# Kernel tuning notes

Measured on AMD Instinct MI355X. Metric: run time of the kernel, lower is better.

The kernel has to match this reference:

```python
import jax, jax.numpy as jnp
import numpy as np

N = 100000   # nodes
E = 1600000  # edges (avg degree 16)
IN = 24
HID = 128
OUT = 12


def setup_inputs() -> dict:
    key = jax.random.key(0)
    ks = jax.random.split(key, 16)
    s = 0.05
    return {
        "inputs": jax.random.normal(ks[0], (N, IN), jnp.float32),
        "src": jax.random.randint(ks[1], (E,), 0, N),
        "dst": jax.random.randint(ks[2], (E,), 0, N),
        "e_w": jax.random.uniform(ks[3], (E, 1), jnp.float32),
        "snorm_n": jax.random.uniform(ks[4], (N, 1), jnp.float32),
        "snorm_e": jax.random.uniform(ks[5], (E, 1), jnp.float32),
        "W_emb": jax.random.normal(ks[6], (IN, HID), jnp.float32) * s,
        "b_emb": jnp.zeros((HID,), jnp.float32),
        "W_self1": jax.random.normal(ks[7], (HID, HID), jnp.float32) * s,
        "W1": jax.random.normal(ks[8], (HID, HID), jnp.float32) * s,
        "b1": jnp.zeros((HID,), jnp.float32),
        "W_self2": jax.random.normal(ks[9], (HID, HID), jnp.float32) * s,
        "W2": jax.random.normal(ks[10], (HID, HID), jnp.float32) * s,
        "b2": jnp.zeros((HID,), jnp.float32),
        "W_fc": jax.random.normal(ks[11], (HID, OUT), jnp.float32) * s,
        "b_fc": jnp.zeros((OUT,), jnp.float32),
    }


def _degrees(src, dst):
    out_deg = jnp.clip(jnp.zeros((N,), jnp.float32).at[src].add(1.0), 1.0)
    in_deg = jnp.clip(jnp.zeros((N,), jnp.float32).at[dst].add(1.0), 1.0)
    return out_deg, in_deg


def _gcn_layer(h, src, dst, e_w, out_deg, in_deg, W_self, W, b):
    # self transform (no bias)
    h_s = h @ W_self
    # source-side symmetric norm, edge-weighted message, sum-aggregate at dst
    feat = h * (out_deg ** -0.5)[:, None]          # [N, H]
    m = feat[src] * e_w                            # [E, H]  u_mul_e
    agg = jax.ops.segment_sum(m, dst, num_segments=N)  # [N, H] sum reduce
    h2 = (agg @ W + b) * (in_deg ** -0.5)[:, None]
    return h_s + h2


def reference(inputs, src, dst, e_w, snorm_n, snorm_e,
              W_emb, b_emb, W_self1, W1, b1, W_self2, W2, b2, W_fc, b_fc):
    out_deg, in_deg = _degrees(src, dst)
    h = inputs @ W_emb + b_emb
    h = jax.nn.relu(_gcn_layer(h, src, dst, e_w, out_deg, in_deg, W_self1, W1, b1))
    h = jax.nn.relu(_gcn_layer(h, src, dst, e_w, out_deg, in_deg, W_self2, W2, b2))
    return h @ W_fc + b_fc
```

## Files before the change

kernel.cpp:

```cpp
#include <hip/hip_runtime.h>

#define NN 100000
#define EE 1600000
#define IN_F 24
#define HID 128
#define OUT_F 12
#define HC 256
#define LBLK 128

#define NBKT 782
#define PA_BLKS 512
#define PA_EPB 3125

#define EMB_B 2048
#define PREP_B 264
#define K1_GRID (PA_BLKS + EMB_B + PREP_B)

typedef unsigned char u8;
typedef unsigned short u16;
typedef unsigned int u32;

using short8 = __attribute__((ext_vector_type(8))) short;
using f32x4  = __attribute__((ext_vector_type(4))) float;

__device__ __forceinline__ float bf2f(u16 h) {
  return __uint_as_float(((u32)h) << 16);
}
__device__ __forceinline__ u16 f2bf(float f) {
  u32 u = __float_as_uint(f);
  u32 r = (u + 0x7FFFu + ((u >> 16) & 1u)) >> 16;
  return (u16)r;
}
__device__ __forceinline__ float inv_sqrt_cnt(int c) {
  if (c < 1) c = 1;
  return 1.0f / sqrtf((float)c);
}

__device__ __forceinline__ void emb_body(int eb, const float* __restrict__ inputs,
                                         const float* __restrict__ W_emb,
                                         const float* __restrict__ b_emb,
                                         u16* __restrict__ hcat, float* smemW) {
  int t = threadIdx.x;
  float* Wls = smemW;
  float* bls = smemW + IN_F * HID;
  for (int i = t; i < IN_F * HID; i += 256) Wls[i] = W_emb[i];
  if (t < HID) bls[t] = b_emb[t];
  __syncthreads();
  int c = t & 127;
  int sub = t >> 7;
  for (int node = eb * 2 + sub; node < NN; node += EMB_B * 2) {
    const float* xr = inputs + (size_t)node * IN_F;
    float acc = bls[c];
    #pragma unroll
    for (int k = 0; k < IN_F; ++k) acc = fmaf(xr[k], Wls[k * HID + c], acc);
    hcat[(size_t)node * HC + c] = f2bf(acc);
  }
}

__device__ __forceinline__ void prep_body(int pb,
    const float* __restrict__ Ws1, const float* __restrict__ W1m,
    const float* __restrict__ Ws2, const float* __restrict__ W2m,
    const float* __restrict__ Wfc,
    u16* __restrict__ WT1, u16* __restrict__ WT2, u16* __restrict__ WfcT) {
  int idx = pb * 256 + (int)threadIdx.x;
  if (idx < 65536) {
    int layer = idx >> 15;
    int rem = idx & 32767;
    int n = rem >> 8, k = rem & 255;
    const float* A = layer ? Ws2 : Ws1;
    const float* B = layer ? W2m : W1m;
    float v = (k < HID) ? A[(size_t)k * HID + n] : B[(size_t)(k - HID) * HID + n];
    (layer ? WT2 : WT1)[(size_t)n * 256 + k] = f2bf(v);
  } else if (idx < 65536 + 2048) {
    int j = idx - 65536;
    int n = j >> 7, k = j & 127;
    WfcT[(size_t)n * 128 + k] = f2bf(n < OUT_F ? Wfc[(size_t)k * OUT_F + n] : 0.f);
  }
}

__global__ __launch_bounds__(256) void k1(
    const int* __restrict__ src, const int* __restrict__ dst,
    u32* __restrict__ histgD, u32* __restrict__ histgS,
    const float* __restrict__ inputs, const float* __restrict__ W_emb,
    const float* __restrict__ b_emb, u16* __restrict__ hcat,
    const float* __restrict__ Ws1, const float* __restrict__ W1m,
    const float* __restrict__ Ws2, const float* __restrict__ W2m,
    const float* __restrict__ Wfc,
    u16* __restrict__ WT1, u16* __restrict__ WT2, u16* __restrict__ WfcT) {
  __shared__ __align__(16) char sm[13312];
  int b = blockIdx.x, t = threadIdx.x;
  if (b < PA_BLKS) {
    u32* histD = (u32*)sm;
    u32* histS = histD + 1024;
    for (int i = t; i < 2048; i += 256) histD[i] = 0;
    __syncthreads();
    int e0 = b * PA_EPB;
    for (int e = e0 + t; e < e0 + PA_EPB; e += 256) {
      atomicAdd(&histD[dst[e] >> 7], 1u);
      atomicAdd(&histS[src[e] >> 7], 1u);
    }
    __syncthreads();
    for (int i = t; i < 1024; i += 256) {
      histgD[(size_t)b * 1024 + i] = histD[i];
      histgS[(size_t)b * 1024 + i] = histS[i];
    }
  } else if (b < PA_BLKS + EMB_B) {
    emb_body(b - PA_BLKS, inputs, W_emb, b_emb, hcat, (float*)sm);
  } else {
    prep_body(b - PA_BLKS - EMB_B, Ws1, W1m, Ws2, W2m, Wfc, WT1, WT2, WfcT);
  }
}

__global__ __launch_bounds__(256) void k_scan1(u32* __restrict__ histgD,
                                               u32* __restrict__ histgS,
                                               u32* __restrict__ totalsD,
                                               u32* __restrict__ totalsS) {
  __shared__ u32 s[512];
  int b = blockIdx.x, t = threadIdx.x;
  u32* hist = (b < NBKT) ? histgD : histgS;
  u32* tot  = (b < NBKT) ? totalsD : totalsS;
  int k = (b < NBKT) ? b : b - NBKT;
  u32 v0 = hist[(size_t)t * 1024 + k];
  u32 v1 = hist[(size_t)(t + 256) * 1024 + k];
  s[t] = v0; s[t + 256] = v1;
  __syncthreads();
  for (int off = 1; off < 512; off <<= 1) {
    u32 a0 = (t >= off) ? s[t - off] : 0;
    u32 a1 = (t + 256 >= off) ? s[t + 256 - off] : 0;
    __syncthreads();
    s[t] += a0; s[t + 256] += a1;
    __syncthreads();
  }
  hist[(size_t)t * 1024 + k] = s[t] - v0;
  hist[(size_t)(t + 256) * 1024 + k] = s[t + 256] - v1;
  if (t == 255) tot[k] = s[511];
}

__global__ __launch_bounds__(1024) void k_scan2(const u32* __restrict__ totalsD,
                                                const u32* __restrict__ totalsS,
                                                u32* __restrict__ estartD,
                                                u32* __restrict__ sstart) {
  __shared__ u32 s[1024];
  const u32* tot = blockIdx.x ? totalsS : totalsD;
  u32* est       = blockIdx.x ? sstart  : estartD;
  int t = threadIdx.x;
  u32 v = (t < NBKT) ? tot[t] : 0;
  s[t] = v;
  __syncthreads();
  for (int off = 1; off < 1024; off <<= 1) {
    u32 a = (t >= off) ? s[t - off] : 0;
    __syncthreads();
    s[t] += a;
    __syncthreads();
  }
  if (t < NBKT) est[t] = s[t] - v;
  if (t == NBKT - 1) est[NBKT] = s[t];
}

__global__ __launch_bounds__(256) void k_passbS(
    const int* __restrict__ src, const u32* __restrict__ histgS,
    const u32* __restrict__ sstart, u8* __restrict__ lo8) {
  __shared__ u32 cur[1024];
  int pb = blockIdx.x, t = threadIdx.x;
  for (int i = t; i < 1024; i += 256)
    cur[i] = ((i < NBKT) ? sstart[i] : 0u) + histgS[(size_t)pb * 1024 + i];
  __syncthreads();
  int e0 = pb * PA_EPB;
  for (int e = e0 + t; e < e0 + PA_EPB; e += 256) {
    int s = src[e];
    u32 pos = atomicAdd(&cur[s >> 7], 1u);
    lo8[pos] = (u8)(s & 127);
  }
}

__global__ __launch_bounds__(256) void k_countS(const u8* __restrict__ lo8,
                                                const u32* __restrict__ sstart,
                                                float* __restrict__ out_norm) {
  __shared__ u32 cnt[128];
  int k = blockIdx.x, t = threadIdx.x;
  if (t < 128) cnt[t] = 0;
  __syncthreads();
  int e0 = (int)sstart[k], e1 = (int)sstart[k + 1];
  for (int e = e0 + t; e < e1; e += 256) atomicAdd(&cnt[lo8[e]], 1u);
  __syncthreads();
  if (t < 128) {
    int node = k * 128 + t;
    if (node < NN) out_norm[node] = inv_sqrt_cnt((int)cnt[t]);
  }
}

__global__ __launch_bounds__(256) void k_passbD(
    const int* __restrict__ src, const int* __restrict__ dst,
    const float* __restrict__ e_w, const float* __restrict__ out_norm,
    const u32* __restrict__ histgD, const u32* __restrict__ estartD,
    u32* __restrict__ csr_stage, u8* __restrict__ dl8) {
  __shared__ u32 cur[1024];
  int pb = blockIdx.x, t = threadIdx.x;
  for (int i = t; i < 1024; i += 256)
    cur[i] = ((i < NBKT) ? estartD[i] : 0u) + histgD[(size_t)pb * 1024 + i];
  __syncthreads();
  int e0 = pb * PA_EPB;
  for (int e = e0 + t; e < e0 + PA_EPB; e += 256) {
    int s = src[e], d = dst[e];
    float w = e_w[e] * out_norm[s];
    u32 pos = atomicAdd(&cur[d >> 7], 1u);
    csr_stage[pos] = (((u32)f2bf(w)) << 17) | (u32)s;
    dl8[pos] = (u8)(d & 127);
  }
}

__global__ __launch_bounds__(256) void k_reorder(
    const u32* __restrict__ csr_stage, const u8* __restrict__ dl8,
    const u32* __restrict__ estart, u32* __restrict__ csr,
    int* __restrict__ row_start, float* __restrict__ in_norm) {
  __shared__ u32 cnt[128], pfx[128], cur[128];
  int k = blockIdx.x, t = threadIdx.x;
  if (t < 128) cnt[t] = 0;
  __syncthreads();
  int e0 = (int)estart[k], e1 = (int)estart[k + 1];
  for (int e = e0 + t; e < e1; e += 256) atomicAdd(&cnt[dl8[e]], 1u);
  __syncthreads();
  if (t < 128) pfx[t] = cnt[t];
  __syncthreads();
  for (int off = 1; off < 128; off <<= 1) {
    u32 v = (t < 128 && t >= off) ? pfx[t - off] : 0;
    __syncthreads();
    if (t < 128) pfx[t] += v;
    __syncthreads();
  }
  if (t < 128) {
    u32 start = (u32)e0 + pfx[t] - cnt[t];
    cur[t] = start;
    int node = k * 128 + t;
    if (node < NN) {
      row_start[node] = (int)start;
      in_norm[node] = inv_sqrt_cnt((int)cnt[t]);
    }
  }
  if (k == NBKT - 1 && t == 0) row_start[NN] = e1;
  __syncthreads();
  for (int e = e0 + t; e < e1; e += 256) {
    u32 pos = atomicAdd(&cur[dl8[e]], 1u);
    csr[pos] = csr_stage[e];
  }
}

__global__ __launch_bounds__(256) void k_agg(const u16* __restrict__ hcat_in,
                                             const int* __restrict__ row_start,
                                             const float* __restrict__ in_norm,
                                             const u32* __restrict__ csr,
                                             u16* __restrict__ hcat_out) {
  int t = threadIdx.x;
  int node = blockIdx.x * 8 + (t >> 5);
  if (node >= NN) return;
  int lane = t & 31;
  int s0 = row_start[node], s1 = row_start[node + 1];
  float ax = 0.f, ay = 0.f, az = 0.f, aw = 0.f;
  for (int i0 = s0; i0 < s1; i0 += 32) {
    u32 pk = 0;
    if (i0 + lane < s1) pk = csr[i0 + lane];
    int m = s1 - i0; if (m > 32) m = 32;
    for (int j = 0; j < m; ++j) {
      u32 p = __shfl(pk, j, 32);
      float w = bf2f((u16)(p >> 17));
      int sv = (int)(p & 0x1FFFF);
      ushort4 hv = *(const ushort4*)(hcat_in + (size_t)sv * HC + lane * 4);
      ax = fmaf(w, bf2f(hv.x), ax);
      ay = fmaf(w, bf2f(hv.y), ay);
      az = fmaf(w, bf2f(hv.z), az);
      aw = fmaf(w, bf2f(hv.w), aw);
    }
  }
  float inn = in_norm[node];
  ushort4 r;
  r.x = f2bf(ax * inn); r.y = f2bf(ay * inn);
  r.z = f2bf(az * inn); r.w = f2bf(aw * inn);
  *(ushort4*)(hcat_out + (size_t)node * HC + HID + lane * 4) = r;
}

template<int FC>
__global__ __launch_bounds__(512) void k_layer(u16* __restrict__ hcat,
    const u16* __restrict__ WT, const float* __restrict__ bias,
    const float* __restrict__ in_norm,
    const u16* __restrict__ WfcT, const float* __restrict__ b_fc,
    float* __restrict__ out) {
  __shared__ char smem[135168];
  const int t = threadIdx.x;
  const int r0 = blockIdx.x * LBLK;

  #pragma unroll
  for (int i = 0; i < 8; ++i) {
    int boff = i * 8192 + t * 16;
    int row = boff >> 9, col = boff & 511;
    uint4 v = *(const uint4*)(hcat + (size_t)(r0 + row) * HC + (col >> 1));
    *(uint4*)(smem + row * 512 + (col ^ ((row & 7) << 4))) = v;
  }
  #pragma unroll
  for (int i = 0; i < 8; ++i) {
    int boff = i * 8192 + t * 16;
    int row = boff >> 9, col = boff & 511;
    uint4 v = *(const uint4*)(WT + (size_t)row * 256 + (col >> 1));
    *(uint4*)(smem + 65536 + row * 512 + (col ^ ((row & 7) << 4))) = v;
  }
  if (FC && t < 256) {
    int row = t >> 4, col = (t & 15) * 16;
    uint4 v = *(const uint4*)(WfcT + (size_t)row * 128 + (col >> 1));
    *(uint4*)(smem + 131072 + row * 256 + (col ^ ((row & 7) << 4))) = v;
  }
  __syncthreads();

  const int lane = t & 63, w = t >> 6;
  const int l15 = lane & 15, lhi = lane >> 4;

  f32x4 acc[8];
  #pragma unroll
  for (int nf = 0; nf < 8; ++nf) acc[nf] = (f32x4){0.f, 0.f, 0.f, 0.f};

  const int arow = w * 16 + l15;
  const char* pa = smem + arow * 512;
  const int aswz = (arow & 7) << 4;
  #pragma unroll
  for (int ks = 0; ks < 8; ++ks) {
    int kb = ks * 64 + (lhi << 4);
    short8 a = *(const short8*)(pa + (kb ^ aswz));
    #pragma unroll
    for (int nf = 0; nf < 8; ++nf) {
      int brow = nf * 16 + l15;
      short8 bf = *(const short8*)(smem + 65536 + brow * 512 + (kb ^ ((brow & 7) << 4)));
      acc[nf] = __builtin_amdgcn_mfma_f32_16x16x32_bf16(a, bf, acc[nf], 0, 0, 0);
    }
  }

  float bcol[8];
  #pragma unroll
  for (int nf = 0; nf < 8; ++nf) bcol[nf] = bias[nf * 16 + l15];

  if (!FC) {
    #pragma unroll
    for (int r = 0; r < 4; ++r) {
      int grow = r0 + w * 16 + (lhi << 2) + r;
      if (grow < NN) {
        float inn = in_norm[grow];
        #pragma unroll
        for (int nf = 0; nf < 8; ++nf) {
          float v = acc[nf][r] + inn * bcol[nf];
          hcat[(size_t)grow * HC + nf * 16 + l15] = f2bf(fmaxf(v, 0.f));
        }
      }
    }
  } else {
    #pragma unroll
    for (int r = 0; r < 4; ++r) {
      int lrow = w * 16 + (lhi << 2) + r;
      int grow = r0 + lrow;
      float inn = (grow < NN) ? in_norm[grow] : 0.f;
      #pragma unroll
      for (int nf = 0; nf < 8; ++nf) {
        int col = nf * 16 + l15;
        float v = fmaxf(acc[nf][r] + inn * bcol[nf], 0.f);
        *(u16*)(smem + lrow * 256 + ((col * 2) ^ ((lrow & 7) << 4))) = f2bf(v);
      }
    }
    __syncthreads();
    f32x4 a2 = (f32x4){0.f, 0.f, 0.f, 0.f};
    const char* pa2 = smem + (w * 16 + l15) * 256;
    const int as2 = (l15 & 7) << 4;
    #pragma unroll
    for (int ks = 0; ks < 4; ++ks) {
      int kb = ks * 64 + (lhi << 4);
      short8 a = *(const short8*)(pa2 + (kb ^ as2));
      short8 bf = *(const short8*)(smem + 131072 + l15 * 256 + (kb ^ as2));
      a2 = __builtin_amdgcn_mfma_f32_16x16x32_bf16(a, bf, a2, 0, 0, 0);
    }
    if (l15 < OUT_F) {
      float bo = b_fc[l15];
      #pragma unroll
      for (int r = 0; r < 4; ++r) {
        int grow = r0 + w * 16 + (lhi << 2) + r;
        if (grow < NN) out[(size_t)grow * OUT_F + l15] = a2[r] + bo;
      }
    }
  }
}

extern "C" void kernel_launch(void* const* d_in, const int* in_sizes, int n_in,
                              void* d_out, int out_size, void* d_ws, size_t ws_size,
                              hipStream_t stream) {
  (void)in_sizes; (void)n_in; (void)out_size;
  const float* inputs  = (const float*)d_in[0];
  const int*   src     = (const int*)d_in[1];
  const int*   dst     = (const int*)d_in[2];
  const float* e_w     = (const float*)d_in[3];
  const float* W_emb   = (const float*)d_in[6];
  const float* b_emb   = (const float*)d_in[7];
  const float* W_self1 = (const float*)d_in[8];
  const float* W1      = (const float*)d_in[9];
  const float* b1      = (const float*)d_in[10];
  const float* W_self2 = (const float*)d_in[11];
  const float* W2      = (const float*)d_in[12];
  const float* b2      = (const float*)d_in[13];
  const float* W_fc    = (const float*)d_in[14];
  const float* b_fc    = (const float*)d_in[15];
  float* out = (float*)d_out;

  u32* histgD      = (u32*)d_ws;
  u32* histgS      = histgD + (size_t)512 * 1024;
  u32* totalsD     = histgS + (size_t)512 * 1024;
  u32* estartD     = totalsD + 1024;
  u32* totalsS     = estartD + 1024;
  u32* sstart      = totalsS + 1024;
  float* out_norm  = (float*)(sstart + 1024);
  float* in_norm   = out_norm + NN;
  int* row_start   = (int*)(in_norm + NN);
  u8* lo8          = (u8*)(row_start + NN + 4);
  u32* csr_stage   = (u32*)(lo8 + EE);
  u32* csr         = csr_stage + EE;
  u16* hcat        = (u16*)(csr + EE);
  u16* WT1         = hcat + (size_t)NN * HC;
  u16* WT2         = WT1 + 32768;
  u16* WfcT        = WT2 + 32768;

  const size_t NEED = (size_t)2 * 512 * 1024 * 4 + 4096 * 4 + (size_t)(3 * NN + 4) * 4
                      + (size_t)EE * 9 + (size_t)NN * HC * 2 + (2 * 32768 + 2048) * 2;
  if (ws_size < NEED) return;

  hipLaunchKernelGGL(k1, dim3(K1_GRID), dim3(256), 0, stream,
                     src, dst, histgD, histgS, inputs, W_emb, b_emb, hcat,
                     W_self1, W1, W_self2, W2, W_fc, WT1, WT2, WfcT);
  hipLaunchKernelGGL(k_scan1, dim3(2 * NBKT), dim3(256), 0, stream,
                     histgD, histgS, totalsD, totalsS);
  hipLaunchKernelGGL(k_scan2, dim3(2), dim3(1024), 0, stream,
                     totalsD, totalsS, estartD, sstart);
  hipLaunchKernelGGL(k_passbS, dim3(PA_BLKS), dim3(256), 0, stream,
                     src, histgS, sstart, lo8);
  hipLaunchKernelGGL(k_countS, dim3(NBKT), dim3(256), 0, stream, lo8, sstart, out_norm);
  hipLaunchKernelGGL(k_passbD, dim3(PA_BLKS), dim3(256), 0, stream,
                     src, dst, e_w, out_norm, histgD, estartD, csr_stage, lo8);
  hipLaunchKernelGGL(k_reorder, dim3(NBKT), dim3(256), 0, stream,
                     csr_stage, lo8, estartD, csr, row_start, in_norm);
  hipLaunchKernelGGL(k_agg, dim3((NN + 7) / 8), dim3(256), 0, stream,
                     hcat, row_start, in_norm, csr, hcat);
  hipLaunchKernelGGL(k_layer<0>, dim3((NN + LBLK - 1) / LBLK), dim3(512), 0, stream,
                     hcat, WT1, b1, in_norm, WfcT, b_fc, out);
  hipLaunchKernelGGL(k_agg, dim3((NN + 7) / 8), dim3(256), 0, stream,
                     hcat, row_start, in_norm, csr, hcat);
  hipLaunchKernelGGL(k_layer<1>, dim3((NN + LBLK - 1) / LBLK), dim3(512), 0, stream,
                     hcat, WT2, b2, in_norm, WfcT, b_fc, out);
}
```

Baseline: 381.0 us.

## Split concatenated feature buffer into separate h and aggregate arrays; unroll gather

Replaces the interleaved [N,256] hcat buffer, which held h and the aggregate side by side, with two dense [N,128] arrays. The gather in k_agg then reads from a compact array with a 256-byte row stride instead of 512, so gathered rows sit closer together and use cache lines better. The gather loop is also unrolled by four so that several independent row loads are in flight at once. k_layer now loads its two halves from the separate arrays into the same swizzled shared layout, which costs an extra pass of address arithmetic but keeps the matmul unchanged.

```diff
diff --git a/kernel.cpp b/kernel.cpp
--- a/kernel.cpp
+++ b/kernel.cpp
@@ -5,7 +5,6 @@
 #define IN_F 24
 #define HID 128
 #define OUT_F 12
-#define HC 256
 #define LBLK 128
 
 #define NBKT 782
@@ -39,7 +38,7 @@
 __device__ __forceinline__ void emb_body(int eb, const float* __restrict__ inputs,
                                          const float* __restrict__ W_emb,
                                          const float* __restrict__ b_emb,
-                                         u16* __restrict__ hcat, float* smemW) {
+                                         u16* __restrict__ harr, float* smemW) {
   int t = threadIdx.x;
   float* Wls = smemW;
   float* bls = smemW + IN_F * HID;
@@ -53,7 +52,7 @@
     float acc = bls[c];
     #pragma unroll
     for (int k = 0; k < IN_F; ++k) acc = fmaf(xr[k], Wls[k * HID + c], acc);
-    hcat[(size_t)node * HC + c] = f2bf(acc);
+    harr[(size_t)node * HID + c] = f2bf(acc);
   }
 }
 
@@ -82,7 +81,7 @@
     const int* __restrict__ src, const int* __restrict__ dst,
     u32* __restrict__ histgD, u32* __restrict__ histgS,
     const float* __restrict__ inputs, const float* __restrict__ W_emb,
-    const float* __restrict__ b_emb, u16* __restrict__ hcat,
+    const float* __restrict__ b_emb, u16* __restrict__ harr,
     const float* __restrict__ Ws1, const float* __restrict__ W1m,
     const float* __restrict__ Ws2, const float* __restrict__ W2m,
     const float* __restrict__ Wfc,
@@ -105,7 +104,7 @@
       histgS[(size_t)b * 1024 + i] = histS[i];
     }
   } else if (b < PA_BLKS + EMB_B) {
-    emb_body(b - PA_BLKS, inputs, W_emb, b_emb, hcat, (float*)sm);
+    emb_body(b - PA_BLKS, inputs, W_emb, b_emb, harr, (float*)sm);
   } else {
     prep_body(b - PA_BLKS - EMB_B, Ws1, W1m, Ws2, W2m, Wfc, WT1, WT2, WfcT);
   }
@@ -245,11 +244,11 @@
   }
 }
 
-__global__ __launch_bounds__(256) void k_agg(const u16* __restrict__ hcat_in,
+__global__ __launch_bounds__(256) void k_agg(const u16* __restrict__ harr,
                                              const int* __restrict__ row_start,
                                              const float* __restrict__ in_norm,
                                              const u32* __restrict__ csr,
-                                             u16* __restrict__ hcat_out) {
+                                             u16* __restrict__ aggr) {
   int t = threadIdx.x;
   int node = blockIdx.x * 8 + (t >> 5);
   if (node >= NN) return;
@@ -260,26 +259,47 @@
     u32 pk = 0;
     if (i0 + lane < s1) pk = csr[i0 + lane];
     int m = s1 - i0; if (m > 32) m = 32;
-    for (int j = 0; j < m; ++j) {
+    int j = 0;
+    for (; j + 4 <= m; j += 4) {
+      u32 p0 = __shfl(pk, j,     32);
+      u32 p1 = __shfl(pk, j + 1, 32);
+      u32 p2 = __shfl(pk, j + 2, 32);
+      u32 p3 = __shfl(pk, j + 3, 32);
+      ushort4 h0 = *(const ushort4*)(harr + (size_t)(p0 & 0x1FFFF) * HID + lane * 4);
+      ushort4 h1 = *(const ushort4*)(harr + (size_t)(p1 & 0x1FFFF) * HID + lane * 4);
+      ushort4 h2 = *(const ushort4*)(harr + (size_t)(p2 & 0x1FFFF) * HID + lane * 4);
+      ushort4 h3 = *(const ushort4*)(harr + (size_t)(p3 & 0x1FFFF) * HID + lane * 4);
+      float w0 = bf2f((u16)(p0 >> 17));
+      float w1 = bf2f((u16)(p1 >> 17));
+      float w2 = bf2f((u16)(p2 >> 17));
+      float w3 = bf2f((u16)(p3 >> 17));
+      ax = fmaf(w0, bf2f(h0.x), ax); ay = fmaf(w0, bf2f(h0.y), ay);
+      az = fmaf(w0, bf2f(h0.z), az); aw = fmaf(w0, bf2f(h0.w), aw);
+      ax = fmaf(w1, bf2f(h1.x), ax); ay = fmaf(w1, bf2f(h1.y), ay);
+      az = fmaf(w1, bf2f(h1.z), az); aw = fmaf(w1, bf2f(h1.w), aw);
+      ax = fmaf(w2, bf2f(h2.x), ax); ay = fmaf(w2, bf2f(h2.y), ay);
+      az = fmaf(w2, bf2f(h2.z), az); aw = fmaf(w2, bf2f(h2.w), aw);
+      ax = fmaf(w3, bf2f(h3.x), ax); ay = fmaf(w3, bf2f(h3.y), ay);
+      az = fmaf(w3, bf2f(h3.z), az); aw = fmaf(w3, bf2f(h3.w), aw);
+    }
+    for (; j < m; ++j) {
       u32 p = __shfl(pk, j, 32);
       float w = bf2f((u16)(p >> 17));
-      int sv = (int)(p & 0x1FFFF);
-      ushort4 hv = *(const ushort4*)(hcat_in + (size_t)sv * HC + lane * 4);
-      ax = fmaf(w, bf2f(hv.x), ax);
-      ay = fmaf(w, bf2f(hv.y), ay);
-      az = fmaf(w, bf2f(hv.z), az);
-      aw = fmaf(w, bf2f(hv.w), aw);
+      ushort4 hv = *(const ushort4*)(harr + (size_t)(p & 0x1FFFF) * HID + lane * 4);
+      ax = fmaf(w, bf2f(hv.x), ax); ay = fmaf(w, bf2f(hv.y), ay);
+      az = fmaf(w, bf2f(hv.z), az); aw = fmaf(w, bf2f(hv.w), aw);
     }
   }
   float inn = in_norm[node];
   ushort4 r;
   r.x = f2bf(ax * inn); r.y = f2bf(ay * inn);
   r.z = f2bf(az * inn); r.w = f2bf(aw * inn);
-  *(ushort4*)(hcat_out + (size_t)node * HC + HID + lane * 4) = r;
+  *(ushort4*)(aggr + (size_t)node * HID + lane * 4) = r;
 }
 
 template<int FC>
-__global__ __launch_bounds__(512) void k_layer(u16* __restrict__ hcat,
+__global__ __launch_bounds__(512) void k_layer(u16* __restrict__ harr,
+    const u16* __restrict__ aggr,
     const u16* __restrict__ WT, const float* __restrict__ bias,
     const float* __restrict__ in_norm,
     const u16* __restrict__ WfcT, const float* __restrict__ b_fc,
@@ -289,11 +309,18 @@
   const int r0 = blockIdx.x * LBLK;
 
   #pragma unroll
-  for (int i = 0; i < 8; ++i) {
+  for (int i = 0; i < 4; ++i) {
     int boff = i * 8192 + t * 16;
-    int row = boff >> 9, col = boff & 511;
-    uint4 v = *(const uint4*)(hcat + (size_t)(r0 + row) * HC + (col >> 1));
+    int row = boff >> 8, col = boff & 255;
+    uint4 v = *(const uint4*)(harr + (size_t)(r0 + row) * HID + (col >> 1));
     *(uint4*)(smem + row * 512 + (col ^ ((row & 7) << 4))) = v;
+  }
+  #pragma unroll
+  for (int i = 0; i < 4; ++i) {
+    int boff = i * 8192 + t * 16;
+    int row = boff >> 8, col = boff & 255;
+    uint4 v = *(const uint4*)(aggr + (size_t)(r0 + row) * HID + (col >> 1));
+    *(uint4*)(smem + row * 512 + (256 + (col ^ ((row & 7) << 4)))) = v;
   }
   #pragma unroll
   for (int i = 0; i < 8; ++i) {
@@ -344,7 +371,7 @@
         #pragma unroll
         for (int nf = 0; nf < 8; ++nf) {
           float v = acc[nf][r] + inn * bcol[nf];
-          hcat[(size_t)grow * HC + nf * 16 + l15] = f2bf(fmaxf(v, 0.f));
+          harr[(size_t)grow * HID + nf * 16 + l15] = f2bf(fmaxf(v, 0.f));
         }
       }
     }
@@ -415,17 +442,18 @@
   u8* lo8          = (u8*)(row_start + NN + 4);
   u32* csr_stage   = (u32*)(lo8 + EE);
   u32* csr         = csr_stage + EE;
-  u16* hcat        = (u16*)(csr + EE);
-  u16* WT1         = hcat + (size_t)NN * HC;
+  u16* harr        = (u16*)(csr + EE);
+  u16* aggr        = harr + (size_t)NN * HID;
+  u16* WT1         = aggr + (size_t)NN * HID;
   u16* WT2         = WT1 + 32768;
   u16* WfcT        = WT2 + 32768;
 
   const size_t NEED = (size_t)2 * 512 * 1024 * 4 + 4096 * 4 + (size_t)(3 * NN + 4) * 4
-                      + (size_t)EE * 9 + (size_t)NN * HC * 2 + (2 * 32768 + 2048) * 2;
+                      + (size_t)EE * 9 + (size_t)NN * HID * 4 + (2 * 32768 + 2048) * 2;
   if (ws_size < NEED) return;
 
   hipLaunchKernelGGL(k1, dim3(K1_GRID), dim3(256), 0, stream,
-                     src, dst, histgD, histgS, inputs, W_emb, b_emb, hcat,
+                     src, dst, histgD, histgS, inputs, W_emb, b_emb, harr,
                      W_self1, W1, W_self2, W2, W_fc, WT1, WT2, WfcT);
   hipLaunchKernelGGL(k_scan1, dim3(2 * NBKT), dim3(256), 0, stream,
                      histgD, histgS, totalsD, totalsS);
@@ -439,11 +467,11 @@
   hipLaunchKernelGGL(k_reorder, dim3(NBKT), dim3(256), 0, stream,
                      csr_stage, lo8, estartD, csr, row_start, in_norm);
   hipLaunchKernelGGL(k_agg, dim3((NN + 7) / 8), dim3(256), 0, stream,
-                     hcat, row_start, in_norm, csr, hcat);
+                     harr, row_start, in_norm, csr, aggr);
   hipLaunchKernelGGL(k_layer<0>, dim3((NN + LBLK - 1) / LBLK), dim3(512), 0, stream,
-                     hcat, WT1, b1, in_norm, WfcT, b_fc, out);
+                     harr, aggr, WT1, b1, in_norm, WfcT, b_fc, out);
   hipLaunchKernelGGL(k_agg, dim3((NN + 7) / 8), dim3(256), 0, stream,
-                     hcat, row_start, in_norm, csr, hcat);
+                     harr, row_start, in_norm, csr, aggr);
   hipLaunchKernelGGL(k_layer<1>, dim3((NN + LBLK - 1) / LBLK), dim3(512), 0, stream,
-                     hcat, WT2, b2, in_norm, WfcT, b_fc, out);
-}
+                     harr, aggr, WT2, b2, in_norm, WfcT, b_fc, out);
+}
```

Measured after the change: 352.8 us. 1.08x faster.
